# Optimization experiments

Hardware: AMD Instinct MI355X
Metric: run time of the kernel (lower is better)

The kernel has to match this reference:

```python
import jax, jax.numpy as jnp
import numpy as np

B, L, D_MODEL, H = 4, 2048, 1024, 16
HD = D_MODEL // H  # head_dim = 64


def _rope_tables(seq_len, dim, dtype):
    inv_freq = 1.0 / (10000.0 ** (jnp.arange(0, dim, 2, dtype=jnp.float32) / dim))
    t = jnp.arange(seq_len, dtype=jnp.float32)
    freqs = jnp.outer(t, inv_freq)  # (S, dim/2)
    return jnp.cos(freqs).astype(dtype), jnp.sin(freqs).astype(dtype)


def _apply_rope(x):
    # x: (B, H, S, d)
    cos, sin = _rope_tables(x.shape[-2], x.shape[-1], x.dtype)  # (S, d/2)
    x_even = x[..., 0::2]
    x_odd = x[..., 1::2]
    out_even = x_even * cos - x_odd * sin
    out_odd = x_even * sin + x_odd * cos
    return jnp.stack([out_even, out_odd], axis=-1).reshape(x.shape)


def setup_inputs() -> dict:
    key = jax.random.key(0)
    ks = jax.random.split(key, 9)
    s = 1.0 / np.sqrt(D_MODEL)
    inp = {
        "query": jax.random.normal(ks[0], (B, L, D_MODEL), dtype=jnp.float32),
        "Wq": jax.random.uniform(ks[1], (D_MODEL, D_MODEL), jnp.float32, -s, s),
        "bq": jax.random.uniform(ks[2], (D_MODEL,), jnp.float32, -s, s),
        "Wk": jax.random.uniform(ks[3], (D_MODEL, D_MODEL), jnp.float32, -s, s),
        "bk": jax.random.uniform(ks[4], (D_MODEL,), jnp.float32, -s, s),
        "Wv": jax.random.uniform(ks[5], (D_MODEL, D_MODEL), jnp.float32, -s, s),
        "bv": jax.random.uniform(ks[6], (D_MODEL,), jnp.float32, -s, s),
        "Wo": jax.random.uniform(ks[7], (D_MODEL, D_MODEL), jnp.float32, -s, s),
        "bo": jax.random.uniform(ks[8], (D_MODEL,), jnp.float32, -s, s),
    }
    return inp


def reference(query, Wq, bq, Wk, bk, Wv, bv, Wo, bo):
    Bq, Lq, _ = query.shape
    # projections (torch Linear: x @ W.T + b), split into heads -> (B, H, L, d)
    def proj(x, W, b):
        y = x @ W.T + b
        return y.reshape(Bq, Lq, H, HD).transpose(0, 2, 1, 3)
    q = _apply_rope(proj(query, Wq, bq))
    k = _apply_rope(proj(query, Wk, bk))
    v = proj(query, Wv, bv)
    scores = jnp.einsum("bhqd,bhkd->bhqk", q, k) / np.sqrt(HD)
    causal_mask = jnp.triu(jnp.ones((Lq, Lq), dtype=bool), k=1)
    scores = jnp.where(causal_mask[None, None, :, :], -jnp.inf, scores)
    attn = jax.nn.softmax(scores, axis=-1)
    out = jnp.einsum("bhqk,bhkd->bhqd", attn, v)
    out = out.transpose(0, 2, 1, 3).reshape(Bq, Lq, D_MODEL)
    return out @ Wo.T + bo
```

## Files before the change

kernel.cpp:

```cpp
#include <hip/hip_runtime.h>
#include <hip/hip_bf16.h>
#include <math.h>

#define L_SEQ  2048
#define DMODEL 1024
#define NHEAD  16
#define HEADD  64

typedef __attribute__((ext_vector_type(8))) short short8;
typedef __attribute__((ext_vector_type(4))) short short4v;
typedef __attribute__((ext_vector_type(4))) float f32x4;

static __device__ __forceinline__ unsigned short f2bf(float f) {
    unsigned int u = __float_as_uint(f);
    unsigned int r = (u + 0x7fffu + ((u >> 16) & 1u)) >> 16;
    return (unsigned short)r;
}

static __device__ __forceinline__ void dma16(const unsigned short* g, unsigned short* l) {
    __builtin_amdgcn_global_load_lds((const __attribute__((address_space(1))) void*)g,
                                     (__attribute__((address_space(3))) void*)l, 16, 0, 0);
}

__global__ void cvt_f32_bf16(const float* __restrict__ in,
                             unsigned short* __restrict__ out, int n4) {
    int i = blockIdx.x * blockDim.x + threadIdx.x;
    if (i >= n4) return;
    float4 v = reinterpret_cast<const float4*>(in)[i];
    ushort4 o;
    o.x = f2bf(v.x); o.y = f2bf(v.y); o.z = f2bf(v.z); o.w = f2bf(v.w);
    reinterpret_cast<ushort4*>(out)[i] = o;
}

__global__ void cvt_weights(const float* __restrict__ Wq, const float* __restrict__ Wk,
                            const float* __restrict__ Wv, const float* __restrict__ Wo,
                            unsigned short* __restrict__ dst) {
    int i = blockIdx.x * blockDim.x + threadIdx.x;
    int which = i >> 18;
    const float* src = which == 0 ? Wq : which == 1 ? Wk : which == 2 ? Wv : Wo;
    float4 v = reinterpret_cast<const float4*>(src)[i & 262143];
    ushort4 o;
    o.x = f2bf(v.x); o.y = f2bf(v.y); o.z = f2bf(v.z); o.w = f2bf(v.w);
    reinterpret_cast<ushort4*>(dst)[i] = o;
}

__global__ void build_rope(float* __restrict__ tab) {
    int i = blockIdx.x * blockDim.x + threadIdx.x;
    int lpos = i >> 5, i2 = i & 31;
    float inv_f = expf(-0.28782313662425574f * (float)i2);
    float ang = (float)lpos * inv_f;
    tab[2 * i]     = cosf(ang);
    tab[2 * i + 1] = sinf(ang);
}

#define BKP 32

__global__ __launch_bounds__(256) void proj_qkv(
    const unsigned short* __restrict__ X,
    const unsigned short* __restrict__ Wqkv,
    const float* __restrict__ bq_,
    const float* __restrict__ bk_,
    const float* __restrict__ bv_,
    const float* __restrict__ rope,
    unsigned short* __restrict__ Qb,
    unsigned short* __restrict__ Kb,
    unsigned short* __restrict__ Vr)
{
    __shared__ unsigned short pool[24576];
    unsigned short* a_ring = pool;
    unsigned short* b_ring = pool + 12288;

    const int tid  = threadIdx.x;
    const int lane = tid & 63;
    const int w    = tid >> 6;
    const int wm   = w & 1, wn = w >> 1;
    const int quad = lane >> 4, l16 = lane & 15;

    const int orig = blockIdx.y * 24 + blockIdx.x;
    const int swz  = (orig & 7) * 192 + (orig >> 3);
    const int bx   = swz % 24;
    const int by   = swz / 24;
    const int m0   = by * 128;
    const int n0   = bx * 128;

    const int sel = bx >> 3;
    const float* bias   = sel == 0 ? bq_ : (sel == 1 ? bk_ : bv_);
    unsigned short* out = sel == 0 ? Qb  : (sel == 1 ? Kb  : Vr);

    const int st_row = lane >> 2;
    const int st_col = (((lane & 3) ^ ((lane >> 3) & 3)) << 3);
    const int rd = ((quad ^ ((l16 >> 1) & 3)) << 3);

    f32x4 acc[4][4];
#pragma unroll
    for (int i = 0; i < 4; ++i)
#pragma unroll
        for (int j = 0; j < 4; ++j) acc[i][j] = (f32x4){0.f, 0.f, 0.f, 0.f};

    const unsigned short* Xs = X    + (size_t)(m0 + w * 32 + st_row) * DMODEL + st_col;
    const unsigned short* Ws = Wqkv + (size_t)(n0 + w * 32 + st_row) * DMODEL + st_col;
    const int ldsA0 = (w * 32) * BKP, ldsA1 = (w * 32 + 16) * BKP;

#pragma unroll
    for (int p = 0; p < 2; ++p) {
        const int kk = p * BKP;
        dma16(Xs + kk,               a_ring + p * 4096 + ldsA0);
        dma16(Xs + 16 * DMODEL + kk, a_ring + p * 4096 + ldsA1);
        dma16(Ws + kk,               b_ring + p * 4096 + ldsA0);
        dma16(Ws + 16 * DMODEL + kk, b_ring + p * 4096 + ldsA1);
    }
    asm volatile("s_waitcnt vmcnt(4)" ::: "memory");
    __builtin_amdgcn_s_barrier();

    for (int kt = 0; kt < 32; ++kt) {
        const int slot = (kt % 3) * 4096;
        const int ps   = ((kt + 2) % 3) * 4096;
        const int kk   = ((kt + 2) & 31) * BKP;

        short8 af[4], bf[2];
#pragma unroll
        for (int i = 0; i < 4; ++i)
            af[i] = *reinterpret_cast<const short8*>(
                &a_ring[slot + (wm * 64 + i * 16 + l16) * BKP + rd]);
#pragma unroll
        for (int j = 0; j < 2; ++j)
            bf[j] = *reinterpret_cast<const short8*>(
                &b_ring[slot + (wn * 64 + j * 16 + l16) * BKP + rd]);
        dma16(Xs + kk,               a_ring + ps + ldsA0);
        dma16(Xs + 16 * DMODEL + kk, a_ring + ps + ldsA1);
        __builtin_amdgcn_s_barrier();
        asm volatile("s_waitcnt lgkmcnt(0)" ::: "memory");
        __builtin_amdgcn_sched_barrier(0);
        __builtin_amdgcn_s_setprio(1);
#pragma unroll
        for (int i = 0; i < 4; ++i)
#pragma unroll
            for (int j = 0; j < 2; ++j)
                acc[i][j] = __builtin_amdgcn_mfma_f32_16x16x32_bf16(af[i], bf[j], acc[i][j], 0, 0, 0);
        __builtin_amdgcn_s_setprio(0);
        __builtin_amdgcn_s_barrier();

#pragma unroll
        for (int j = 0; j < 2; ++j)
            bf[j] = *reinterpret_cast<const short8*>(
                &b_ring[slot + (wn * 64 + (2 + j) * 16 + l16) * BKP + rd]);
        dma16(Ws + kk,               b_ring + ps + ldsA0);
        dma16(Ws + 16 * DMODEL + kk, b_ring + ps + ldsA1);
        __builtin_amdgcn_s_barrier();
        asm volatile("s_waitcnt lgkmcnt(0)" ::: "memory");
        __builtin_amdgcn_sched_barrier(0);
        __builtin_amdgcn_s_setprio(1);
#pragma unroll
        for (int i = 0; i < 4; ++i)
#pragma unroll
            for (int j = 0; j < 2; ++j)
                acc[i][2 + j] = __builtin_amdgcn_mfma_f32_16x16x32_bf16(af[i], bf[j], acc[i][2 + j], 0, 0, 0);
        __builtin_amdgcn_s_setprio(0);
        asm volatile("s_waitcnt vmcnt(4)" ::: "memory");
        __builtin_amdgcn_s_barrier();
    }
    asm volatile("s_waitcnt vmcnt(0)" ::: "memory");
    __builtin_amdgcn_s_barrier();

#pragma unroll
    for (int jf = 0; jf < 4; ++jf) {
        int nl = wn * 64 + jf * 16 + l16;
        int nn = (bx & 7) * 128 + nl;
        float bval = bias[nn];
        int d  = nn & (HEADD - 1);
        float sgn = (d & 1) ? 1.0f : -1.0f;
        int i2 = d >> 1;
#pragma unroll
        for (int mf = 0; mf < 4; ++mf) {
#pragma unroll
            for (int r = 0; r < 4; ++r) {
                int ml = wm * 64 + mf * 16 + quad * 4 + r;
                int lpos = (m0 + ml) & (L_SEQ - 1);
                float v = acc[mf][jf][r] + bval;
                if (sel < 2) {
                    float p = __shfl_xor(v, 1);
                    float2 cs = *reinterpret_cast<const float2*>(&rope[(size_t)(lpos * 32 + i2) * 2]);
                    v = v * cs.x + sgn * cs.y * p;
                    if (sel == 0) v *= 0.18033688011112042f;
                }
                pool[(sel < 2) ? (ml * 136 + nl) : (nl * 136 + ml)] = f2bf(v);
            }
        }
    }
    __builtin_amdgcn_s_barrier();

    const int b     = m0 >> 11;
    const int lpos0 = m0 & (L_SEQ - 1);
#pragma unroll
    for (int i = 0; i < 8; ++i) {
        int g   = i * 256 + tid;
        int row = g >> 4;
        int c8  = (g & 15) * 8;
        int4 val = *reinterpret_cast<const int4*>(&pool[row * 136 + c8]);
        size_t addr;
        if (sel < 2) {
            int n_g = (bx & 7) * 128 + c8;
            int h = n_g >> 6, d = n_g & 63;
            addr = ((size_t)(b * NHEAD + h) * L_SEQ + (lpos0 + row)) * HEADD + d;
        } else {
            int n_g = (bx & 7) * 128 + row;
            int h = n_g >> 6, d = n_g & 63;
            addr = ((size_t)(b * NHEAD + h) * HEADD + d) * L_SEQ + lpos0 + c8;
        }
        *reinterpret_cast<int4*>(out + addr) = val;
    }
}

__global__ __launch_bounds__(256) void attn_fwd(
    const unsigned short* __restrict__ Q,
    const unsigned short* __restrict__ K,
    const unsigned short* __restrict__ Vt,
    unsigned short* __restrict__ Oa)
{
    __shared__ unsigned short k_lds[2][64 * 64];
    __shared__ unsigned short v_lds[2][64 * 64];
    const int tid  = threadIdx.x;
    const int lane = tid & 63;
    const int w    = tid >> 6;
    const int quad = lane >> 4, l16 = lane & 15;
    const int pair = blockIdx.y;
    const int bh   = blockIdx.x;
    const size_t base = (size_t)bh * L_SEQ * HEADD;
    const int b = bh >> 4, h = bh & 15;

    const int srow  = lane >> 3;
    const int sslot = lane & 7;
    const int ssw   = ((sslot ^ srow) << 3);
    const unsigned short* Ksrc = K  + base + (size_t)(w * 8 + srow) * HEADD + ssw;
    const unsigned short* Vsrc = Vt + base + (size_t)(w * 8 + srow) * L_SEQ + ssw;
    const int d0 = (w * 8) * 64;
    const int d1 = (32 + w * 8) * 64;
    const int swr = (l16 & 7);

    for (int half = 0; half < 2; ++half) {
        const int s = half ? (15 - pair) : pair;
        const int qrow0 = s * 128 + w * 16 + l16;
        const int qrow1 = qrow0 + 64;
        const int kbmax = 2 * s + 1;

        short8 qf0[2], qf1[2];
#pragma unroll
        for (int ks = 0; ks < 2; ++ks) {
            qf0[ks] = *reinterpret_cast<const short8*>(Q + base + (size_t)qrow0 * HEADD + ks * 32 + quad * 8);
            qf1[ks] = *reinterpret_cast<const short8*>(Q + base + (size_t)qrow1 * HEADD + ks * 32 + quad * 8);
        }

        f32x4 o0[4], o1[4];
#pragma unroll
        for (int nt = 0; nt < 4; ++nt) {
            o0[nt] = (f32x4){0.f, 0.f, 0.f, 0.f};
            o1[nt] = (f32x4){0.f, 0.f, 0.f, 0.f};
        }
        float lsum0 = 0.f, lsum1 = 0.f;

        dma16(Ksrc,                 &k_lds[0][d0]);
        dma16(Ksrc + 32 * HEADD,    &k_lds[0][d1]);
        dma16(Vsrc,                 &v_lds[0][d0]);
        dma16(Vsrc + 32 * L_SEQ,    &v_lds[0][d1]);
        asm volatile("s_waitcnt vmcnt(0)" ::: "memory");
        __builtin_amdgcn_s_barrier();

        int cur = 0;
        for (int kb = 0; kb <= kbmax; ++kb) {
            const int kn = (kb + 1) <= kbmax ? (kb + 1) : 0;
            const int nb = cur ^ 1;
            dma16(Ksrc + (size_t)(kn * 64) * HEADD,        &k_lds[nb][d0]);
            dma16(Ksrc + (size_t)(kn * 64 + 32) * HEADD,   &k_lds[nb][d1]);
            dma16(Vsrc + kn * 64,                          &v_lds[nb][d0]);
            dma16(Vsrc + kn * 64 + 32 * L_SEQ,             &v_lds[nb][d1]);

            f32x4 st0[4], st1[4];
#pragma unroll
            for (int nt = 0; nt < 4; ++nt) {
                st0[nt] = (f32x4){0.f, 0.f, 0.f, 0.f};
                st1[nt] = (f32x4){0.f, 0.f, 0.f, 0.f};
            }
            __builtin_amdgcn_s_setprio(1);
#pragma unroll
            for (int ks = 0; ks < 2; ++ks)
#pragma unroll
                for (int nt = 0; nt < 4; ++nt) {
                    short8 kf = *reinterpret_cast<const short8*>(
                        &k_lds[cur][(nt * 16 + l16) * 64 + (((ks * 4 + quad) ^ swr) << 3)]);
                    st0[nt] = __builtin_amdgcn_mfma_f32_16x16x32_bf16(kf, qf0[ks], st0[nt], 0, 0, 0);
                    st1[nt] = __builtin_amdgcn_mfma_f32_16x16x32_bf16(kf, qf1[ks], st1[nt], 0, 0, 0);
                }
            __builtin_amdgcn_s_setprio(0);

            if (kb >= 2 * s) {
#pragma unroll
                for (int nt = 0; nt < 4; ++nt)
#pragma unroll
                    for (int r = 0; r < 4; ++r) {
                        int seqcol = kb * 64 + nt * 16 + quad * 4 + r;
                        if (seqcol > qrow0) st0[nt][r] = -INFINITY;
                    }
            }
            if (kb == kbmax) {
#pragma unroll
                for (int nt = 0; nt < 4; ++nt)
#pragma unroll
                    for (int r = 0; r < 4; ++r) {
                        int seqcol = kb * 64 + nt * 16 + quad * 4 + r;
                        if (seqcol > qrow1) st1[nt][r] = -INFINITY;
                    }
            }

            short4v pfrag0[4], pfrag1[4];
#pragma unroll
            for (int nt = 0; nt < 4; ++nt) {
                float p0 = __builtin_amdgcn_exp2f(st0[nt][0]);
                float p1 = __builtin_amdgcn_exp2f(st0[nt][1]);
                float p2 = __builtin_amdgcn_exp2f(st0[nt][2]);
                float p3 = __builtin_amdgcn_exp2f(st0[nt][3]);
                lsum0 += (p0 + p1) + (p2 + p3);
                unsigned u0 = __float_as_uint(p0) + 0x8000u;
                unsigned u1 = __float_as_uint(p1) + 0x8000u;
                unsigned u2 = __float_as_uint(p2) + 0x8000u;
                unsigned u3 = __float_as_uint(p3) + 0x8000u;
                union { unsigned u[2]; short4v v; } pk;
                pk.u[0] = (u0 >> 16) | (u1 & 0xffff0000u);
                pk.u[1] = (u2 >> 16) | (u3 & 0xffff0000u);
                pfrag0[nt] = pk.v;

                float q0e = __builtin_amdgcn_exp2f(st1[nt][0]);
                float q1e = __builtin_amdgcn_exp2f(st1[nt][1]);
                float q2e = __builtin_amdgcn_exp2f(st1[nt][2]);
                float q3e = __builtin_amdgcn_exp2f(st1[nt][3]);
                lsum1 += (q0e + q1e) + (q2e + q3e);
                unsigned v0 = __float_as_uint(q0e) + 0x8000u;
                unsigned v1 = __float_as_uint(q1e) + 0x8000u;
                unsigned v2 = __float_as_uint(q2e) + 0x8000u;
                unsigned v3 = __float_as_uint(q3e) + 0x8000u;
                union { unsigned u[2]; short4v v; } pk1;
                pk1.u[0] = (v0 >> 16) | (v1 & 0xffff0000u);
                pk1.u[1] = (v2 >> 16) | (v3 & 0xffff0000u);
                pfrag1[nt] = pk1.v;
            }

            __builtin_amdgcn_s_setprio(1);
#pragma unroll
            for (int c = 0; c < 4; ++c)
#pragma unroll
                for (int nt2 = 0; nt2 < 4; ++nt2) {
                    short4v vf = *reinterpret_cast<const short4v*>(
                        &v_lds[cur][(nt2 * 16 + l16) * 64 +
                                    (((c * 2 + (quad >> 1)) ^ swr) << 3) + ((quad & 1) << 2)]);
                    o0[nt2] = __builtin_amdgcn_mfma_f32_16x16x16bf16_1k(pfrag0[c], vf, o0[nt2], 0, 0, 0);
                    o1[nt2] = __builtin_amdgcn_mfma_f32_16x16x16bf16_1k(pfrag1[c], vf, o1[nt2], 0, 0, 0);
                }
            __builtin_amdgcn_s_setprio(0);

            asm volatile("s_waitcnt vmcnt(0)" ::: "memory");
            __builtin_amdgcn_s_barrier();
            cur ^= 1;
        }

        lsum0 += __shfl_xor(lsum0, 16);
        lsum0 += __shfl_xor(lsum0, 32);
        lsum1 += __shfl_xor(lsum1, 16);
        lsum1 += __shfl_xor(lsum1, 32);
        float rs0[4], rs1[4];
#pragma unroll
        for (int r = 0; r < 4; ++r) {
            rs0[r] = __shfl(lsum0, quad * 4 + r);
            rs1[r] = __shfl(lsum1, quad * 4 + r);
        }
#pragma unroll
        for (int r = 0; r < 4; ++r) {
            float inv0 = 1.0f / rs0[r];
            float inv1 = 1.0f / rs1[r];
            int lg0 = s * 128 + w * 16 + quad * 4 + r;
            int lg1 = lg0 + 64;
#pragma unroll
            for (int nt = 0; nt < 4; ++nt) {
                int d = nt * 16 + l16;
                Oa[(size_t)(b * L_SEQ + lg0) * DMODEL + h * HEADD + d] = f2bf(o0[nt][r] * inv0);
                Oa[(size_t)(b * L_SEQ + lg1) * DMODEL + h * HEADD + d] = f2bf(o1[nt][r] * inv1);
            }
        }
    }
}

__global__ __launch_bounds__(256) void out_gemm(
    const unsigned short* __restrict__ X,
    const unsigned short* __restrict__ W,
    const float* __restrict__ bias,
    float* __restrict__ out)
{
    __shared__ unsigned short a_lds[3][128 * BKP];
    __shared__ unsigned short b_lds[3][128 * BKP];
    const int tid  = threadIdx.x;
    const int lane = tid & 63;
    const int w    = tid >> 6;
    const int wm   = w & 1, wn = w >> 1;
    const int quad = lane >> 4, l16 = lane & 15;

    const int orig = blockIdx.y * 8 + blockIdx.x;
    const int swz  = (orig & 7) * 64 + (orig >> 3);
    const int m0 = (swz >> 3) * 128;
    const int n0 = (swz & 7) * 128;

    const int st_row = lane >> 2;
    const int st_col = (((lane & 3) ^ ((lane >> 3) & 3)) << 3);
    const int rd = ((quad ^ ((l16 >> 1) & 3)) << 3);

    f32x4 acc[4][4];
#pragma unroll
    for (int i = 0; i < 4; ++i)
#pragma unroll
        for (int j = 0; j < 4; ++j) acc[i][j] = (f32x4){0.f, 0.f, 0.f, 0.f};

    const unsigned short* Xs = X + (size_t)(m0 + w * 32 + st_row) * DMODEL + st_col;
    const unsigned short* Ws = W + (size_t)(n0 + w * 32 + st_row) * DMODEL + st_col;
    const int ldsA0 = (w * 32) * BKP, ldsA1 = (w * 32 + 16) * BKP;

#pragma unroll
    for (int p = 0; p < 2; ++p) {
        const int kk = p * BKP;
        dma16(Xs + kk,               &a_lds[p][ldsA0]);
        dma16(Xs + 16 * DMODEL + kk, &a_lds[p][ldsA1]);
        dma16(Ws + kk,               &b_lds[p][ldsA0]);
        dma16(Ws + 16 * DMODEL + kk, &b_lds[p][ldsA1]);
    }
    asm volatile("s_waitcnt vmcnt(4)" ::: "memory");
    __builtin_amdgcn_s_barrier();

    for (int kt = 0; kt < 32; ++kt) {
        const int slot = kt % 3;
        const int ps   = (kt + 2) % 3;
        const int kk   = ((kt + 2) & 31) * BKP;

        dma16(Xs + kk,               &a_lds[ps][ldsA0]);
        dma16(Xs + 16 * DMODEL + kk, &a_lds[ps][ldsA1]);
        dma16(Ws + kk,               &b_lds[ps][ldsA0]);
        dma16(Ws + 16 * DMODEL + kk, &b_lds[ps][ldsA1]);

        short8 af[4], bf[4];
#pragma unroll
        for (int i = 0; i < 4; ++i)
            af[i] = *reinterpret_cast<const short8*>(
                &a_lds[slot][(wm * 64 + i * 16 + l16) * BKP + rd]);
#pragma unroll
        for (int j = 0; j < 4; ++j)
            bf[j] = *reinterpret_cast<const short8*>(
                &b_lds[slot][(wn * 64 + j * 16 + l16) * BKP + rd]);
        asm volatile("s_waitcnt lgkmcnt(0)" ::: "memory");
        __builtin_amdgcn_sched_barrier(0);
        __builtin_amdgcn_s_setprio(1);
#pragma unroll
        for (int i = 0; i < 4; ++i)
#pragma unroll
            for (int j = 0; j < 4; ++j)
                acc[i][j] = __builtin_amdgcn_mfma_f32_16x16x32_bf16(af[i], bf[j], acc[i][j], 0, 0, 0);
        __builtin_amdgcn_s_setprio(0);
        asm volatile("s_waitcnt vmcnt(4)" ::: "memory");
        __builtin_amdgcn_s_barrier();
    }
    asm volatile("s_waitcnt vmcnt(0)" ::: "memory");

#pragma unroll
    for (int nt = 0; nt < 4; ++nt) {
        int n_g = n0 + wn * 64 + nt * 16 + l16;
        float bv = bias[n_g];
#pragma unroll
        for (int mt = 0; mt < 4; ++mt)
#pragma unroll
            for (int r = 0; r < 4; ++r) {
                int m_g = m0 + wm * 64 + mt * 16 + quad * 4 + r;
                out[(size_t)m_g * DMODEL + n_g] = acc[mt][nt][r] + bv;
            }
    }
}

extern "C" void kernel_launch(void* const* d_in, const int* in_sizes, int n_in,
                              void* d_out, int out_size, void* d_ws, size_t ws_size,
                              hipStream_t stream) {
    const float* query = (const float*)d_in[0];
    const float* Wq = (const float*)d_in[1];
    const float* bq = (const float*)d_in[2];
    const float* Wk = (const float*)d_in[3];
    const float* bk = (const float*)d_in[4];
    const float* Wv = (const float*)d_in[5];
    const float* bv = (const float*)d_in[6];
    const float* Wo = (const float*)d_in[7];
    const float* bo = (const float*)d_in[8];
    float* out = (float*)d_out;

    unsigned short* ws  = (unsigned short*)d_ws;
    unsigned short* xb  = ws;
    unsigned short* wqb = xb  + (size_t)8388608;
    unsigned short* wkb = wqb + 1048576;
    unsigned short* wvb = wkb + 1048576;
    unsigned short* wob = wvb + 1048576;
    unsigned short* Qb  = wob + 1048576;
    unsigned short* Kb  = Qb  + 8388608;
    unsigned short* Vr  = Kb  + 8388608;
    unsigned short* Ab  = Vr  + 8388608;
    float* rope = (float*)(Ab + 8388608);

    (void)wkb; (void)wvb;

    build_rope<<<256, 256, 0, stream>>>(rope);
    cvt_f32_bf16<<<8192, 256, 0, stream>>>(query, xb, 2097152);
    cvt_weights<<<4096, 256, 0, stream>>>(Wq, Wk, Wv, Wo, wqb);

    proj_qkv<<<dim3(24, 64), 256, 0, stream>>>(xb, wqb, bq, bk, bv, rope, Qb, Kb, Vr);
    attn_fwd<<<dim3(64, 8), 256, 0, stream>>>(Qb, Kb, Vr, Ab);
    out_gemm<<<dim3(8, 64), 256, 0, stream>>>(Ab, wob, bo, out);
}
```

Measured before the change: 283.8 us.

## Fuse conversion and RoPE prep kernels and remap GEMM tiles per XCD

Three preprocessing kernels (input bf16 conversion, weight conversion, RoPE table build) become one `prep` launch. It dispatches on global thread id to cut two kernel launches and their tail gaps. Both GEMM kernels also change their block-to-tile mapping. Each XCD now takes a contiguous band of 8 row tiles and walks across column tiles, so A-operand rows stay hot in that XCD's L2. The new mapping changes the B-operand reuse pattern, and the merged kernel mixes divergent work types within one grid.

```diff
diff --git a/kernel.cpp b/kernel.cpp
--- a/kernel.cpp
+++ b/kernel.cpp
@@ -22,35 +22,35 @@
                                      (__attribute__((address_space(3))) void*)l, 16, 0, 0);
 }
 
-__global__ void cvt_f32_bf16(const float* __restrict__ in,
-                             unsigned short* __restrict__ out, int n4) {
-    int i = blockIdx.x * blockDim.x + threadIdx.x;
-    if (i >= n4) return;
-    float4 v = reinterpret_cast<const float4*>(in)[i];
-    ushort4 o;
-    o.x = f2bf(v.x); o.y = f2bf(v.y); o.z = f2bf(v.z); o.w = f2bf(v.w);
-    reinterpret_cast<ushort4*>(out)[i] = o;
-}
-
-__global__ void cvt_weights(const float* __restrict__ Wq, const float* __restrict__ Wk,
-                            const float* __restrict__ Wv, const float* __restrict__ Wo,
-                            unsigned short* __restrict__ dst) {
-    int i = blockIdx.x * blockDim.x + threadIdx.x;
-    int which = i >> 18;
-    const float* src = which == 0 ? Wq : which == 1 ? Wk : which == 2 ? Wv : Wo;
-    float4 v = reinterpret_cast<const float4*>(src)[i & 262143];
-    ushort4 o;
-    o.x = f2bf(v.x); o.y = f2bf(v.y); o.z = f2bf(v.z); o.w = f2bf(v.w);
-    reinterpret_cast<ushort4*>(dst)[i] = o;
-}
-
-__global__ void build_rope(float* __restrict__ tab) {
-    int i = blockIdx.x * blockDim.x + threadIdx.x;
-    int lpos = i >> 5, i2 = i & 31;
-    float inv_f = expf(-0.28782313662425574f * (float)i2);
-    float ang = (float)lpos * inv_f;
-    tab[2 * i]     = cosf(ang);
-    tab[2 * i + 1] = sinf(ang);
+__global__ __launch_bounds__(256) void prep(
+    const float* __restrict__ query,
+    const float* __restrict__ Wq, const float* __restrict__ Wk,
+    const float* __restrict__ Wv, const float* __restrict__ Wo,
+    unsigned short* __restrict__ xb, unsigned short* __restrict__ wdst,
+    float* __restrict__ rope)
+{
+    int gid = blockIdx.x * 256 + threadIdx.x;
+    if (gid < 2097152) {
+        float4 v = reinterpret_cast<const float4*>(query)[gid];
+        ushort4 o;
+        o.x = f2bf(v.x); o.y = f2bf(v.y); o.z = f2bf(v.z); o.w = f2bf(v.w);
+        reinterpret_cast<ushort4*>(xb)[gid] = o;
+    } else if (gid < 2097152 + 1048576) {
+        int i = gid - 2097152;
+        int which = i >> 18;
+        const float* src = which == 0 ? Wq : which == 1 ? Wk : which == 2 ? Wv : Wo;
+        float4 v = reinterpret_cast<const float4*>(src)[i & 262143];
+        ushort4 o;
+        o.x = f2bf(v.x); o.y = f2bf(v.y); o.z = f2bf(v.z); o.w = f2bf(v.w);
+        reinterpret_cast<ushort4*>(wdst)[i] = o;
+    } else if (gid < 2097152 + 1048576 + 65536) {
+        int i = gid - (2097152 + 1048576);
+        int lpos = i >> 5, i2 = i & 31;
+        float inv_f = expf(-0.28782313662425574f * (float)i2);
+        float ang = (float)lpos * inv_f;
+        rope[2 * i]     = cosf(ang);
+        rope[2 * i + 1] = sinf(ang);
+    }
 }
 
 #define BKP 32
@@ -77,9 +77,10 @@
     const int quad = lane >> 4, l16 = lane & 15;
 
     const int orig = blockIdx.y * 24 + blockIdx.x;
-    const int swz  = (orig & 7) * 192 + (orig >> 3);
-    const int bx   = swz % 24;
-    const int by   = swz / 24;
+    const int xcd  = orig & 7;
+    const int k    = orig >> 3;
+    const int by   = xcd * 8 + (k & 7);
+    const int bx   = k >> 3;
     const int m0   = by * 128;
     const int n0   = bx * 128;
 
@@ -402,9 +403,10 @@
     const int quad = lane >> 4, l16 = lane & 15;
 
     const int orig = blockIdx.y * 8 + blockIdx.x;
-    const int swz  = (orig & 7) * 64 + (orig >> 3);
-    const int m0 = (swz >> 3) * 128;
-    const int n0 = (swz & 7) * 128;
+    const int xcd  = orig & 7;
+    const int k    = orig >> 3;
+    const int m0   = (xcd * 8 + (k & 7)) * 128;
+    const int n0   = (k >> 3) * 128;
 
     const int st_row = lane >> 2;
     const int st_col = (((lane & 3) ^ ((lane >> 3) & 3)) << 3);
@@ -506,9 +508,7 @@
 
     (void)wkb; (void)wvb;
 
-    build_rope<<<256, 256, 0, stream>>>(rope);
-    cvt_f32_bf16<<<8192, 256, 0, stream>>>(query, xb, 2097152);
-    cvt_weights<<<4096, 256, 0, stream>>>(Wq, Wk, Wv, Wo, wqb);
+    prep<<<12545, 256, 0, stream>>>(query, Wq, Wk, Wv, Wo, xb, wqb, rope);
 
     proj_qkv<<<dim3(24, 64), 256, 0, stream>>>(xb, wqb, bq, bk, bv, rope, Qb, Kb, Vr);
     attn_fwd<<<dim3(64, 8), 256, 0, stream>>>(Qb, Kb, Vr, Ab);
```

After: 272.0 us. 4.1% less time.
